# Kernel tuning notes

Measured on AMD Instinct MI355X. Metric: run time of the kernel, lower is better.

The kernel has to match this reference:

```python
import jax, jax.numpy as jnp
import numpy as np

L = 2048
E = 1024
H = 16
D = E // H


def setup_inputs() -> dict:
    key = jax.random.key(0)
    ks = jax.random.split(key, 9)
    inp = {
        "values": jax.random.normal(ks[0], (L, E), dtype=jnp.float32),
        "keys": jax.random.normal(ks[1], (L, E), dtype=jnp.float32),
        "query": jax.random.normal(ks[2], (L, E), dtype=jnp.float32),
        "dist_matrix": jax.random.uniform(ks[3], (L, L), dtype=jnp.float32),
        "Wv": jax.random.normal(ks[4], (E, E), dtype=jnp.float32) * 0.02,
        "Wk": jax.random.normal(ks[5], (E, E), dtype=jnp.float32) * 0.02,
        "Wq": jax.random.normal(ks[6], (E, E), dtype=jnp.float32) * 0.02,
        "Wo": jax.random.normal(ks[7], (E, E), dtype=jnp.float32) * 0.02,
        "bo": jax.random.normal(ks[8], (E,), dtype=jnp.float32) * 0.02,
    }
    return inp


def reference(values, keys, query, dist_matrix, Wv, Wk, Wq, Wo, bo):
    # Linear projections (torch Linear: x @ W.T), then split heads: [L, H, D]
    v = (values @ Wv.T).reshape(L, H, D)
    k = (keys @ Wk.T).reshape(L, H, D)
    q = (query @ Wq.T).reshape(L, H, D)

    # energy: [H, Lq, Lk]
    energy = jnp.einsum("qhd,khd->hqk", q, k)

    # distance bias: zeros -> inf, then 1/(d+1); broadcast over heads
    dm = jnp.where(dist_matrix == 0, jnp.inf, dist_matrix)
    bias = 1.0 / (dm + 1.0)
    energy = energy + bias[None, :, :]

    attn = jax.nn.softmax(energy / jnp.sqrt(jnp.float32(E)), axis=2)

    out = jnp.einsum("hql,lhd->qhd", attn, v).reshape(L, H * D)
    return out @ Wo.T + bo
```

## Files before the change

kernel.cpp:

```cpp
#include <hip/hip_runtime.h>


#define L_SEQ 2048
#define E_DIM 1024
#define H_HEADS 16
#define D_HEAD 64
#define KSPLIT 4
#define OSPLIT 4

typedef unsigned short u16;
typedef unsigned int u32;
typedef __attribute__((ext_vector_type(8))) short bf16x8;
typedef __attribute__((ext_vector_type(8))) unsigned short u16x8;
typedef __attribute__((ext_vector_type(4))) unsigned short u16x4;
typedef __attribute__((ext_vector_type(4))) float f32x4;

#define C_LOG2E_32 0.045084220027780106f

__device__ __forceinline__ float bf2f(u16 u) {
  union { u32 i; float f; } v; v.i = ((u32)u) << 16; return v.f;
}
__device__ __forceinline__ u16 f2bf(float f) {
  union { float f; u32 i; } v; v.f = f;
  u32 u = v.i;
  u += 0x7FFFu + ((u >> 16) & 1u);
  return (u16)(u >> 16);
}
__device__ __forceinline__ u32 pack_bf16_pair(float lo, float hi) {
  union { float f; u32 u; } a, b;
  a.f = lo; b.f = hi;
  return __builtin_amdgcn_perm(b.u + 0x8000u, a.u + 0x8000u, 0x07060302u);
}
__device__ __forceinline__ void gload16(const u16* g, u16* l) {
  __builtin_amdgcn_global_load_lds(
      (const __attribute__((address_space(1))) u32*)g,
      (__attribute__((address_space(3))) u32*)l, 16, 0, 0);
}

__global__ void cvt_all(const float* __restrict__ xq, const float* __restrict__ xk,
                        const float* __restrict__ xv,
                        const float* __restrict__ wq, const float* __restrict__ wk,
                        const float* __restrict__ wv, const float* __restrict__ wo,
                        const float* __restrict__ dist, const float* __restrict__ bo,
                        u16* oq, u16* ok, u16* ov,
                        u16* owq, u16* owk, u16* owv, u16* owo, u16* obias,
                        float* __restrict__ outp)
{
  size_t gid = (size_t)blockIdx.x * 256 + threadIdx.x;
  const size_t NQ = 262144;
  const size_t NW = 131072;
  const size_t DL = 524288;
  const size_t FILL = 3 * NQ + 4 * NW + DL;

  if (gid >= FILL) {
    size_t off = (gid - FILL) * 8;
    int n = (int)(off & (E_DIM - 1));
    *(f32x4*)&outp[off] = *(const f32x4*)&bo[n];
    *(f32x4*)&outp[off + 4] = *(const f32x4*)&bo[n + 4];
    return;
  }

  const float* src; u16* dst; size_t off; bool isb = false;
  if      (gid <     NQ)           { src = xq;   dst = oq;    off = gid; }
  else if (gid < 2 * NQ)           { src = xk;   dst = ok;    off = gid - NQ; }
  else if (gid < 3 * NQ)           { src = xv;   dst = ov;    off = gid - 2 * NQ; }
  else if (gid < 3 * NQ + NW)      { src = wq;   dst = owq;   off = gid - 3 * NQ; }
  else if (gid < 3 * NQ + 2 * NW)  { src = wk;   dst = owk;   off = gid - 3 * NQ - NW; }
  else if (gid < 3 * NQ + 3 * NW)  { src = wv;   dst = owv;   off = gid - 3 * NQ - 2 * NW; }
  else if (gid < 3 * NQ + 4 * NW)  { src = wo;   dst = owo;   off = gid - 3 * NQ - 3 * NW; }
  else { src = dist; dst = obias; off = gid - 3 * NQ - 4 * NW; isb = true; }

  f32x4 v0 = *(const f32x4*)&src[off * 8];
  f32x4 v1 = *(const f32x4*)&src[off * 8 + 4];
  u16x8 o;
#pragma unroll
  for (int j = 0; j < 4; ++j) {
    float f0 = v0[j], f1 = v1[j];
    if (isb) {
      f0 = (f0 == 0.f) ? 0.f : C_LOG2E_32 / (f0 + 1.f);
      f1 = (f1 == 0.f) ? 0.f : C_LOG2E_32 / (f1 + 1.f);
    }
    o[j] = f2bf(f0); o[j + 4] = f2bf(f1);
  }
  *(u16x8*)&dst[off * 8] = o;
}

#define TM 128
#define TN 128
#define BK 32

template<int OUTMODE>
__global__ __launch_bounds__(256, 3) void gemm_pd(
    const u16* __restrict__ A0, const u16* __restrict__ B0, void* __restrict__ C0,
    const u16* __restrict__ A1, const u16* __restrict__ B1, void* __restrict__ C1,
    const u16* __restrict__ A2, const u16* __restrict__ B2, void* __restrict__ C2,
    int M, int N, int K)
{
  const u16* A; const u16* B; void* C;
  if (OUTMODE == 2)         { A = A0; B = B0; C = C0; }
  else if (blockIdx.z == 0) { A = A0; B = B0; C = C0; }
  else if (blockIdx.z == 1) { A = A1; B = B1; C = C1; }
  else                      { A = A2; B = B2; C = C2; }

  __shared__ __align__(16) u16 As[2][TM * BK];
  __shared__ __align__(16) u16 Bs[2][TN * BK];

  const int m0 = blockIdx.y * TM;
  const int n0 = blockIdx.x * TN;
  const int t = threadIdx.x;
  const int wave = t >> 6;
  const int lane = t & 63;
  const int quad = lane >> 4;
  const int col  = lane & 15;
  const int wm = (wave >> 1) * 64;
  const int wn = (wave & 1) * 64;

  const int sr = lane >> 2;
  const int sg = ((lane & 3) ^ ((lane >> 3) & 3)) * 8;
  const u16* gA = A + (size_t)(m0 + wave * 32 + sr) * K + sg;
  const u16* gB = B + (size_t)(n0 + wave * 32 + sr) * K + sg;
  const int lo0 = (wave * 32) * BK;
  const int lo1 = (wave * 32 + 16) * BK;

  const int kbeg = (OUTMODE == 2) ? blockIdx.z * (K / OSPLIT) : 0;
  const int kend = (OUTMODE == 2) ? kbeg + K / OSPLIT : K;

  f32x4 acc[4][4];
#pragma unroll
  for (int i = 0; i < 4; ++i)
#pragma unroll
    for (int j = 0; j < 4; ++j) acc[i][j] = (f32x4){0.f, 0.f, 0.f, 0.f};

  gload16(gA + kbeg, &As[0][lo0]);
  gload16(gA + (size_t)16 * K + kbeg, &As[0][lo1]);
  gload16(gB + kbeg, &Bs[0][lo0]);
  gload16(gB + (size_t)16 * K + kbeg, &Bs[0][lo1]);

  const int slot8 = (quad ^ ((col >> 1) & 3)) * 8;

  int buf = 0;
  for (int k0 = kbeg; k0 < kend; k0 += BK) {
    __syncthreads();
    int nk = k0 + BK;
    if (nk < kend) {
      gload16(gA + nk, &As[buf ^ 1][lo0]);
      gload16(gA + (size_t)16 * K + nk, &As[buf ^ 1][lo1]);
      gload16(gB + nk, &Bs[buf ^ 1][lo0]);
      gload16(gB + (size_t)16 * K + nk, &Bs[buf ^ 1][lo1]);
    }

    bf16x8 af[4], bfr[4];
#pragma unroll
    for (int i = 0; i < 4; ++i)
      af[i] = *(const bf16x8*)&As[buf][(wm + i * 16 + col) * BK + slot8];
#pragma unroll
    for (int j = 0; j < 4; ++j)
      bfr[j] = *(const bf16x8*)&Bs[buf][(wn + j * 16 + col) * BK + slot8];

#pragma unroll
    for (int i = 0; i < 4; ++i)
#pragma unroll
      for (int j = 0; j < 4; ++j)
        acc[i][j] = __builtin_amdgcn_mfma_f32_16x16x32_bf16(af[i], bfr[j], acc[i][j], 0, 0, 0);

    buf ^= 1;
  }

  const bool transC = (OUTMODE == 0) && (blockIdx.z == 2);
#pragma unroll
  for (int i = 0; i < 4; ++i) {
    int rowb = m0 + wm + i * 16 + quad * 4;
#pragma unroll
    for (int j = 0; j < 4; ++j) {
      int cn = n0 + wn + j * 16 + col;
      if (OUTMODE == 2) {
#pragma unroll
        for (int r = 0; r < 4; ++r)
          unsafeAtomicAdd(&((float*)C)[(size_t)(rowb + r) * N + cn], acc[i][j][r]);
      } else if (transC) {
        u16x4 pk;
#pragma unroll
        for (int r = 0; r < 4; ++r) pk[r] = f2bf(acc[i][j][r]);
        *(u16x4*)&((u16*)C)[(size_t)cn * M + rowb] = pk;
      } else {
#pragma unroll
        for (int r = 0; r < 4; ++r)
          ((u16*)C)[(size_t)(rowb + r) * N + cn] = f2bf(acc[i][j][r]);
      }
    }
  }
}

#define FK 32
#define PLDV 40

__global__ __launch_bounds__(512, 2) void flash7(
    const u16* __restrict__ Q, const u16* __restrict__ Kp,
    const u16* __restrict__ Vt, const u16* __restrict__ Bb,
    u16* __restrict__ Op, float* __restrict__ lp)
{
  __shared__ __align__(16) u16 Ks[2][FK * 64];
  __shared__ __align__(16) u16 Vs[2][D_HEAD * FK];
  __shared__ __align__(16) u16 Ps[8][2][16][PLDV];

  const int h  = blockIdx.y;
  const int q0 = blockIdx.x * 256;
  const int z  = blockIdx.z;
  const int hoff = h * D_HEAD;
  const int kbase = z * (L_SEQ / KSPLIT);
  const int NT = (L_SEQ / KSPLIT) / FK;
  const int t = threadIdx.x;
  const int wave = t >> 6;
  const int lane = t & 63;
  const int quad = lane >> 4;
  const int col  = lane & 15;

  bf16x8 qf[2][2];
  const u16* brow[2];
#pragma unroll
  for (int s = 0; s < 2; ++s) {
    const int qs = q0 + wave * 32 + s * 16;
    const u16* qrow = Q + (size_t)(qs + col) * E_DIM + hoff;
    qf[s][0] = *(const bf16x8*)(qrow + quad * 8);
    qf[s][1] = *(const bf16x8*)(qrow + 32 + quad * 8);
    brow[s] = Bb + (size_t)(qs + col) * L_SEQ;
  }

  const bool isK = (wave < 4);
  const int kq = wave & 3;
  const int krow = kq * 8 + (lane >> 3);
  const int kg = ((lane & 7) ^ (lane >> 3)) * 8;
  const u16* gK = Kp + (size_t)krow * E_DIM + hoff + kg;
  const int vrow = kq * 16 + (lane >> 2);
  const int vg = ((lane & 3) ^ ((lane >> 4) & 3)) * 8;
  const u16* gV = Vt + (size_t)(hoff + vrow) * L_SEQ + vg;

  float l_lane[2] = {0.f, 0.f};
  f32x4 oacc[2][4];
#pragma unroll
  for (int s = 0; s < 2; ++s)
#pragma unroll
    for (int td = 0; td < 4; ++td) oacc[s][td] = (f32x4){0.f, 0.f, 0.f, 0.f};

  if (isK) gload16(gK + (size_t)kbase * E_DIM, &Ks[0][kq * 8 * 64]);
  else     gload16(gV + kbase, &Vs[0][kq * 16 * FK]);
  u16x4 bv[2][2], bn[2][2];
#pragma unroll
  for (int s = 0; s < 2; ++s) {
    bv[s][0] = *(const u16x4*)&brow[s][kbase + quad * 4];
    bv[s][1] = *(const u16x4*)&brow[s][kbase + 16 + quad * 4];
  }

  const int ks0 = (quad ^ (col & 7)) * 8;
  const int ks1 = ((quad + 4) ^ (col & 7)) * 8;
  const int vsl = (quad ^ ((col >> 2) & 3)) * 8;

  int buf = 0;
  for (int kt = 0; kt < NT; ++kt) {
    const int k0 = kbase + kt * FK;
    __syncthreads();
    if (kt + 1 < NT) {
      const int nk = k0 + FK;
      if (isK) gload16(gK + (size_t)nk * E_DIM, &Ks[buf ^ 1][kq * 8 * 64]);
      else     gload16(gV + nk, &Vs[buf ^ 1][kq * 16 * FK]);
#pragma unroll
      for (int s = 0; s < 2; ++s) {
        bn[s][0] = *(const u16x4*)&brow[s][nk + quad * 4];
        bn[s][1] = *(const u16x4*)&brow[s][nk + 16 + quad * 4];
      }
    }
    const u16* Kb = &Ks[buf][0];
    const u16* Vb = &Vs[buf][0];

#pragma unroll
    for (int tt = 0; tt < 2; ++tt) {
      const u16* kr = &Kb[(tt * 16 + col) * 64];
      bf16x8 kf0 = *(const bf16x8*)&kr[ks0];
      bf16x8 kf1 = *(const bf16x8*)&kr[ks1];
#pragma unroll
      for (int s = 0; s < 2; ++s) {
        f32x4 a = (f32x4){0.f, 0.f, 0.f, 0.f};
        a = __builtin_amdgcn_mfma_f32_16x16x32_bf16(kf0, qf[s][0], a, 0, 0, 0);
        a = __builtin_amdgcn_mfma_f32_16x16x32_bf16(kf1, qf[s][1], a, 0, 0, 0);
        float p[4];
#pragma unroll
        for (int r = 0; r < 4; ++r) {
          p[r] = __builtin_amdgcn_exp2f(fmaf(a[r], C_LOG2E_32, bf2f(bv[s][tt][r])));
          l_lane[s] += p[r];
        }
        uint2 w;
        w.x = pack_bf16_pair(p[0], p[1]);
        w.y = pack_bf16_pair(p[2], p[3]);
        *(uint2*)&Ps[wave][s][col][tt * 16 + quad * 4] = w;
      }
    }

#pragma unroll
    for (int s = 0; s < 2; ++s) {
      bf16x8 pf = *(const bf16x8*)&Ps[wave][s][col][quad * 8];
#pragma unroll
      for (int td = 0; td < 4; ++td) {
        bf16x8 vf = *(const bf16x8*)&Vb[(td * 16 + col) * FK + vsl];
        oacc[s][td] = __builtin_amdgcn_mfma_f32_16x16x32_bf16(pf, vf, oacc[s][td], 0, 0, 0);
      }
    }

#pragma unroll
    for (int s = 0; s < 2; ++s) { bv[s][0] = bn[s][0]; bv[s][1] = bn[s][1]; }
    buf ^= 1;
  }

#pragma unroll
  for (int s = 0; s < 2; ++s) {
    l_lane[s] += __shfl_xor(l_lane[s], 16);
    l_lane[s] += __shfl_xor(l_lane[s], 32);
    if (lane < 16)
      lp[((size_t)z * L_SEQ + q0 + wave * 32 + s * 16 + lane) * H_HEADS + h] = l_lane[s];
  }

#pragma unroll
  for (int s = 0; s < 2; ++s) {
    const int qrow_mine = q0 + wave * 32 + s * 16 + quad * 4;
#pragma unroll
    for (int td = 0; td < 4; ++td)
#pragma unroll
      for (int r = 0; r < 4; ++r)
        Op[((size_t)z * L_SEQ + qrow_mine + r) * E_DIM + hoff + td * 16 + col] = f2bf(oacc[s][td][r]);
  }
}

__global__ void merge_attn(const u16* __restrict__ Op, const float* __restrict__ lp,
                           u16* __restrict__ AOb)
{
  size_t gid = (size_t)blockIdx.x * 256 + threadIdx.x;
  size_t idx = gid * 4;
  int q = (int)(idx >> 10);
  int e = (int)(idx & 1023);
  int h = e >> 6;
  float o[4] = {0.f, 0.f, 0.f, 0.f};
  float lsum = 0.f;
#pragma unroll
  for (int s = 0; s < KSPLIT; ++s) {
    u16x4 pv = *(const u16x4*)&Op[((size_t)s * L_SEQ + q) * E_DIM + e];
#pragma unroll
    for (int j = 0; j < 4; ++j) o[j] += bf2f(pv[j]);
    lsum += lp[((size_t)s * L_SEQ + q) * H_HEADS + h];
  }
  float inv = 1.f / lsum;
  u16x4 pk;
#pragma unroll
  for (int j = 0; j < 4; ++j) pk[j] = f2bf(o[j] * inv);
  *(u16x4*)&AOb[idx] = pk;
}

extern "C" void kernel_launch(void* const* d_in, const int* in_sizes, int n_in,
                              void* d_out, int out_size, void* d_ws, size_t ws_size,
                              hipStream_t stream)
{
  const float* values = (const float*)d_in[0];
  const float* keys   = (const float*)d_in[1];
  const float* query  = (const float*)d_in[2];
  const float* dist   = (const float*)d_in[3];
  const float* Wv     = (const float*)d_in[4];
  const float* Wk     = (const float*)d_in[5];
  const float* Wq     = (const float*)d_in[6];
  const float* Wo     = (const float*)d_in[7];
  const float* bo     = (const float*)d_in[8];
  float* out = (float*)d_out;

  const size_t MB = (size_t)1 << 20;
  char* w = (char*)d_ws;
  u16* xq  = (u16*)(w + 0 * MB);
  u16* xk  = (u16*)(w + 4 * MB);
  u16* xv  = (u16*)(w + 8 * MB);
  u16* wqb = (u16*)(w + 12 * MB);
  u16* wkb = (u16*)(w + 14 * MB);
  u16* wvb = (u16*)(w + 16 * MB);
  u16* wob = (u16*)(w + 18 * MB);
  u16* Bb  = (u16*)(w + 20 * MB);
  u16* Qh  = (u16*)(w + 28 * MB);
  u16* Kh  = (u16*)(w + 32 * MB);
  u16* Vth = (u16*)(w + 36 * MB);
  u16* AOb = (u16*)(w + 40 * MB);
  float* lp = (float*)(w + 44 * MB);
  u16* Op  = (u16*)(w + 0 * MB);

  cvt_all<<<8192, 256, 0, stream>>>(query, keys, values, Wq, Wk, Wv, Wo, dist, bo,
                                    xq, xk, xv, wqb, wkb, wvb, wob, Bb, out);

  dim3 gProj(E_DIM / TN, L_SEQ / TM, 3);
  gemm_pd<0><<<gProj, 256, 0, stream>>>(xq, wqb, Qh,
                                        xk, wkb, Kh,
                                        xv, wvb, Vth,
                                        L_SEQ, E_DIM, E_DIM);

  dim3 gAttn(L_SEQ / 256, H_HEADS, KSPLIT);
  flash7<<<gAttn, 512, 0, stream>>>(Qh, Kh, Vth, Bb, Op, lp);

  merge_attn<<<(L_SEQ * E_DIM / 4) / 256, 256, 0, stream>>>(Op, lp, AOb);

  dim3 gOut(E_DIM / TN, L_SEQ / TM, OSPLIT);
  gemm_pd<2><<<gOut, 256, 0, stream>>>(AOb, wob, out,
                                       AOb, wob, out,
                                       AOb, wob, out,
                                       L_SEQ, E_DIM, E_DIM);
}
```

Measured before the change: 213.0 us.

## Load GEMM A operand directly to registers, halve out-proj split, narrow convert vectors

The projection and output GEMMs now read the A tile straight from global memory into registers with a one-step register prefetch, instead of staging it through LDS. This halves shared memory use and raises the occupancy hint from 3 to 4. The output GEMM K-split drops from 4 to 2, which halves the atomic adds at the cost of fewer blocks. The conversion kernel handles 4 elements per thread instead of 8, using twice as many blocks. The direct A loads have each lane fetch 16 bytes from rows K elements apart, which may coalesce worse and expose global latency.

Result: slower. 218.3 us (+2.5%).

```diff
diff --git a/kernel.cpp b/kernel.cpp
--- a/kernel.cpp
+++ b/kernel.cpp
@@ -6,7 +6,7 @@
 #define H_HEADS 16
 #define D_HEAD 64
 #define KSPLIT 4
-#define OSPLIT 4
+#define OSPLIT 2
 
 typedef unsigned short u16;
 typedef unsigned int u32;
@@ -47,16 +47,15 @@
                         float* __restrict__ outp)
 {
   size_t gid = (size_t)blockIdx.x * 256 + threadIdx.x;
-  const size_t NQ = 262144;
-  const size_t NW = 131072;
-  const size_t DL = 524288;
+  const size_t NQ = 524288;
+  const size_t NW = 262144;
+  const size_t DL = 1048576;
   const size_t FILL = 3 * NQ + 4 * NW + DL;
 
   if (gid >= FILL) {
-    size_t off = (gid - FILL) * 8;
+    size_t off = (gid - FILL) * 4;
     int n = (int)(off & (E_DIM - 1));
     *(f32x4*)&outp[off] = *(const f32x4*)&bo[n];
-    *(f32x4*)&outp[off + 4] = *(const f32x4*)&bo[n + 4];
     return;
   }
 
@@ -70,19 +69,15 @@
   else if (gid < 3 * NQ + 4 * NW)  { src = wo;   dst = owo;   off = gid - 3 * NQ - 3 * NW; }
   else { src = dist; dst = obias; off = gid - 3 * NQ - 4 * NW; isb = true; }
 
-  f32x4 v0 = *(const f32x4*)&src[off * 8];
-  f32x4 v1 = *(const f32x4*)&src[off * 8 + 4];
-  u16x8 o;
+  f32x4 v = *(const f32x4*)&src[off * 4];
+  u16x4 o;
 #pragma unroll
   for (int j = 0; j < 4; ++j) {
-    float f0 = v0[j], f1 = v1[j];
-    if (isb) {
-      f0 = (f0 == 0.f) ? 0.f : C_LOG2E_32 / (f0 + 1.f);
-      f1 = (f1 == 0.f) ? 0.f : C_LOG2E_32 / (f1 + 1.f);
-    }
-    o[j] = f2bf(f0); o[j + 4] = f2bf(f1);
-  }
-  *(u16x8*)&dst[off * 8] = o;
+    float f = v[j];
+    if (isb) f = (f == 0.f) ? 0.f : C_LOG2E_32 / (f + 1.f);
+    o[j] = f2bf(f);
+  }
+  *(u16x4*)&dst[off * 4] = o;
 }
 
 #define TM 128
@@ -90,7 +85,7 @@
 #define BK 32
 
 template<int OUTMODE>
-__global__ __launch_bounds__(256, 3) void gemm_pd(
+__global__ __launch_bounds__(256, 4) void gemm_rd(
     const u16* __restrict__ A0, const u16* __restrict__ B0, void* __restrict__ C0,
     const u16* __restrict__ A1, const u16* __restrict__ B1, void* __restrict__ C1,
     const u16* __restrict__ A2, const u16* __restrict__ B2, void* __restrict__ C2,
@@ -102,7 +97,6 @@
   else if (blockIdx.z == 1) { A = A1; B = B1; C = C1; }
   else                      { A = A2; B = B2; C = C2; }
 
-  __shared__ __align__(16) u16 As[2][TM * BK];
   __shared__ __align__(16) u16 Bs[2][TN * BK];
 
   const int m0 = blockIdx.y * TM;
@@ -117,11 +111,12 @@
 
   const int sr = lane >> 2;
   const int sg = ((lane & 3) ^ ((lane >> 3) & 3)) * 8;
-  const u16* gA = A + (size_t)(m0 + wave * 32 + sr) * K + sg;
   const u16* gB = B + (size_t)(n0 + wave * 32 + sr) * K + sg;
   const int lo0 = (wave * 32) * BK;
   const int lo1 = (wave * 32 + 16) * BK;
 
+  const u16* gA = A + (size_t)(m0 + wm + col) * K + quad * 8;
+
   const int kbeg = (OUTMODE == 2) ? blockIdx.z * (K / OSPLIT) : 0;
   const int kend = (OUTMODE == 2) ? kbeg + K / OSPLIT : K;
 
@@ -131,10 +126,12 @@
 #pragma unroll
     for (int j = 0; j < 4; ++j) acc[i][j] = (f32x4){0.f, 0.f, 0.f, 0.f};
 
-  gload16(gA + kbeg, &As[0][lo0]);
-  gload16(gA + (size_t)16 * K + kbeg, &As[0][lo1]);
   gload16(gB + kbeg, &Bs[0][lo0]);
   gload16(gB + (size_t)16 * K + kbeg, &Bs[0][lo1]);
+  bf16x8 af[4], an[4];
+#pragma unroll
+  for (int i = 0; i < 4; ++i)
+    af[i] = *(const bf16x8*)(gA + (size_t)(i * 16) * K + kbeg);
 
   const int slot8 = (quad ^ ((col >> 1) & 3)) * 8;
 
@@ -143,16 +140,14 @@
     __syncthreads();
     int nk = k0 + BK;
     if (nk < kend) {
-      gload16(gA + nk, &As[buf ^ 1][lo0]);
-      gload16(gA + (size_t)16 * K + nk, &As[buf ^ 1][lo1]);
       gload16(gB + nk, &Bs[buf ^ 1][lo0]);
       gload16(gB + (size_t)16 * K + nk, &Bs[buf ^ 1][lo1]);
+#pragma unroll
+      for (int i = 0; i < 4; ++i)
+        an[i] = *(const bf16x8*)(gA + (size_t)(i * 16) * K + nk);
     }
 
-    bf16x8 af[4], bfr[4];
-#pragma unroll
-    for (int i = 0; i < 4; ++i)
-      af[i] = *(const bf16x8*)&As[buf][(wm + i * 16 + col) * BK + slot8];
+    bf16x8 bfr[4];
 #pragma unroll
     for (int j = 0; j < 4; ++j)
       bfr[j] = *(const bf16x8*)&Bs[buf][(wn + j * 16 + col) * BK + slot8];
@@ -163,6 +158,8 @@
       for (int j = 0; j < 4; ++j)
         acc[i][j] = __builtin_amdgcn_mfma_f32_16x16x32_bf16(af[i], bfr[j], acc[i][j], 0, 0, 0);
 
+#pragma unroll
+    for (int i = 0; i < 4; ++i) af[i] = an[i];
     buf ^= 1;
   }
 
@@ -385,11 +382,11 @@
   float* lp = (float*)(w + 44 * MB);
   u16* Op  = (u16*)(w + 0 * MB);
 
-  cvt_all<<<8192, 256, 0, stream>>>(query, keys, values, Wq, Wk, Wv, Wo, dist, bo,
-                                    xq, xk, xv, wqb, wkb, wvb, wob, Bb, out);
+  cvt_all<<<16384, 256, 0, stream>>>(query, keys, values, Wq, Wk, Wv, Wo, dist, bo,
+                                     xq, xk, xv, wqb, wkb, wvb, wob, Bb, out);
 
   dim3 gProj(E_DIM / TN, L_SEQ / TM, 3);
-  gemm_pd<0><<<gProj, 256, 0, stream>>>(xq, wqb, Qh,
+  gemm_rd<0><<<gProj, 256, 0, stream>>>(xq, wqb, Qh,
                                         xk, wkb, Kh,
                                         xv, wvb, Vth,
                                         L_SEQ, E_DIM, E_DIM);
@@ -400,7 +397,7 @@
   merge_attn<<<(L_SEQ * E_DIM / 4) / 256, 256, 0, stream>>>(Op, lp, AOb);
 
   dim3 gOut(E_DIM / TN, L_SEQ / TM, OSPLIT);
-  gemm_pd<2><<<gOut, 256, 0, stream>>>(AOb, wob, out,
+  gemm_rd<2><<<gOut, 256, 0, stream>>>(AOb, wob, out,
                                        AOb, wob, out,
                                        AOb, wob, out,
                                        L_SEQ, E_DIM, E_DIM);
```
